# Kernel optimization log

Measured on AMD Instinct MI355X. Metric: run time of the kernel, lower is better.

Reference implementation:

```python
import jax, jax.numpy as jnp
import numpy as np
from jax import lax

B, S, K, H, NCLS = 64, 2048, 2, 256, 2
D = K * K  # input_dim = conv_kernel ** 2


def setup_inputs() -> dict:
    key = jax.random.key(0)
    ks = jax.random.split(key, 12)
    s = 0.1
    return {
        "x": jax.random.normal(ks[0], (B, S, D), dtype=jnp.float32),
        # elementwise quanvolution-style conv filter (k x k)
        "conv_w": jax.random.normal(ks[1], (K, K), dtype=jnp.float32) * s,
        "conv_b": jax.random.normal(ks[2], (K, K), dtype=jnp.float32) * s,
        # LSTM params, torch gate order (i, f, g, o)
        "w_ih": jax.random.normal(ks[3], (4 * H, D), dtype=jnp.float32) * s,
        "w_hh": jax.random.normal(ks[4], (4 * H, H), dtype=jnp.float32) * s,
        "b_ih": jax.random.normal(ks[5], (4 * H,), dtype=jnp.float32) * s,
        "b_hh": jax.random.normal(ks[6], (4 * H,), dtype=jnp.float32) * s,
        # classifier: depth=2 ReLU layers + final Linear(H, NCLS)
        "w1": jax.random.normal(ks[7], (H, H), dtype=jnp.float32) * s,
        "b1": jnp.zeros((H,), dtype=jnp.float32),
        "w2": jax.random.normal(ks[8], (H, H), dtype=jnp.float32) * s,
        "b2": jnp.zeros((H,), dtype=jnp.float32),
        "w3": jax.random.normal(ks[9], (NCLS, H), dtype=jnp.float32) * s,
        "b3": jnp.zeros((NCLS,), dtype=jnp.float32),
    }


def _lstm(feat, w_ih, w_hh, b_ih, b_hh):
    # feat: [B, S, D] -> hidden states [B, S, H]
    b, _, _ = feat.shape
    h_dim = w_hh.shape[1]
    bias = b_ih + b_hh
    # precompute input projections for all timesteps (batched GEMM)
    gates_x = jnp.einsum('bsd,gd->bsg', feat, w_ih) + bias  # [B, S, 4H]

    def step(carry, gx):
        h, c = carry
        gates = gx + h @ w_hh.T  # [B, 4H]
        i, f, g, o = jnp.split(gates, 4, axis=-1)
        i, f, o = jax.nn.sigmoid(i), jax.nn.sigmoid(f), jax.nn.sigmoid(o)
        g = jnp.tanh(g)
        c = f * c + i * g
        h = o * jnp.tanh(c)
        return (h, c), h

    init = (jnp.zeros((b, h_dim), feat.dtype), jnp.zeros((b, h_dim), feat.dtype))
    _, hs = lax.scan(step, init, gates_x.transpose(1, 0, 2))  # hs: [S, B, H]
    return hs.transpose(1, 0, 2)


def reference(x, conv_w, conv_b, w_ih, w_hh, b_ih, b_hh, w1, b1, w2, b2, w3, b3):
    b, s, _ = x.shape
    # batched replacement of the per-patch CPU conv loop
    patches = x.reshape(b, s, K, K)
    feat = jax.nn.sigmoid(patches * conv_w + conv_b).reshape(b, s, K * K)
    lstm_out = _lstm(feat, w_ih, w_hh, b_ih, b_hh)  # [B, S, H]
    h1 = jax.nn.relu(lstm_out @ w1.T + b1)
    h2 = jax.nn.relu(h1 @ w2.T + b2)
    logits = h2 @ w3.T + b3  # [B, S, NCLS]
    return logits
```

## Files before the change

kernel.cpp:

```cpp
#include <hip/hip_runtime.h>


#define BB 64
#define SS 2048
#define HH 256

typedef _Float16 f16;
typedef _Float16 h2 __attribute__((ext_vector_type(2)));
typedef _Float16 v8h __attribute__((ext_vector_type(8)));

union V8H { v8h v; h2 p[4]; };

__device__ __forceinline__ float fdot2f(h2 a, h2 b, float c){
#if __has_builtin(__builtin_amdgcn_fdot2)
  return __builtin_amdgcn_fdot2(a, b, c, false);
#else
  return c + (float)a.x*(float)b.x + (float)a.y*(float)b.y;
#endif
}

__device__ __forceinline__ float qsum4(float x){
#if __has_builtin(__builtin_amdgcn_mov_dpp)
  x += __int_as_float(__builtin_amdgcn_mov_dpp(__float_as_int(x), 0xB1, 0xf, 0xf, true));
  x += __int_as_float(__builtin_amdgcn_mov_dpp(__float_as_int(x), 0x4E, 0xf, 0xf, true));
#else
  x += __shfl_xor(x, 1, 64);
  x += __shfl_xor(x, 2, 64);
#endif
  return x;
}

__device__ __forceinline__ float rcpf_(float x){
#if __has_builtin(__builtin_amdgcn_rcpf)
  return __builtin_amdgcn_rcpf(x);
#else
  return 1.f/x;
#endif
}
__device__ __forceinline__ float sigmf_(float x){ return rcpf_(1.f + __expf(-x)); }
__device__ __forceinline__ float tanhf_(float x){
  x = fminf(fmaxf(x, -15.f), 15.f);
  float e = __expf(2.f*x);
  return (e - 1.f)*rcpf_(e + 1.f);
}
__device__ __forceinline__ h2 mkh2(float a, float b){ h2 r; r.x=(f16)a; r.y=(f16)b; return r; }

__device__ __forceinline__ void lds_barrier(){
  asm volatile("s_waitcnt lgkmcnt(0)\n\ts_barrier" ::: "memory");
}

__global__ void prep_kernel(
    const float* __restrict__ x, const float* __restrict__ conv_w, const float* __restrict__ conv_b,
    const float* __restrict__ w_ih, const float* __restrict__ w_hh,
    const float* __restrict__ b_ih, const float* __restrict__ b_hh,
    const float* __restrict__ w1, const float* __restrict__ w2, const float* __restrict__ w3,
    f16* __restrict__ feat2, f16* __restrict__ wstream, f16* __restrict__ wihp,
    float* __restrict__ biasp, f16* __restrict__ w1t, f16* __restrict__ w2t, f16* __restrict__ w3p)
{
  int id = blockIdx.x*256 + threadIdx.x;
  if (id < BB*SS){
    float4 xv = *(const float4*)(x + (size_t)id*4);
    float f0 = sigmf_(xv.x*conv_w[0] + conv_b[0]);
    float f1 = sigmf_(xv.y*conv_w[1] + conv_b[1]);
    float f2 = sigmf_(xv.z*conv_w[2] + conv_b[2]);
    float f3 = sigmf_(xv.w*conv_w[3] + conv_b[3]);
    h2* o = (h2*)feat2 + (size_t)id*2;
    o[0] = mkh2(f0,f1); o[1] = mkh2(f2,f3);
    return;
  }
  id -= BB*SS;
  if (id < 8192){
    int c = id >> 10, t = id & 1023;
    int u = t >> 2, kq = t & 3;
    int row = 768 + u;
    int j0 = kq*64 + c*8;
    const float* src = w_hh + (size_t)row*256 + j0;
    v8h o;
    #pragma unroll
    for (int j=0;j<8;j++) o[j] = (f16)src[j];
    *((v8h*)wstream + (size_t)c*1024 + t) = o;
    return;
  }
  id -= 8192;
  if (id < 1024){
    int u = id >> 2;
    f16* o = wihp + (size_t)id*16;
    float bb[4];
    #pragma unroll
    for (int i=0;i<4;i++){
      int row = u + 256*i;
      o[i*4+0] = (f16)w_ih[row*4+0];
      o[i*4+1] = (f16)w_ih[row*4+1];
      o[i*4+2] = (f16)w_ih[row*4+2];
      o[i*4+3] = (f16)w_ih[row*4+3];
      bb[i] = b_ih[row] + b_hh[row];
    }
    *(float4*)(biasp + (size_t)id*4) = make_float4(bb[0],bb[1],bb[2],bb[3]);
    return;
  }
  id -= 1024;
  if (id < 32768){
    int kp = id >> 8, n = id & 255;
    w1t[(size_t)id*2+0] = (f16)w1[(size_t)n*256 + 2*kp];
    w1t[(size_t)id*2+1] = (f16)w1[(size_t)n*256 + 2*kp+1];
    return;
  }
  id -= 32768;
  if (id < 32768){
    int kp = id >> 8, n = id & 255;
    w2t[(size_t)id*2+0] = (f16)w2[(size_t)n*256 + 2*kp];
    w2t[(size_t)id*2+1] = (f16)w2[(size_t)n*256 + 2*kp+1];
    return;
  }
  id -= 32768;
  if (id < 256){
    int kp = id >> 1, cls = id & 1;
    w3p[(size_t)id*2+0] = (f16)w3[(size_t)cls*256 + 2*kp];
    w3p[(size_t)id*2+1] = (f16)w3[(size_t)cls*256 + 2*kp+1];
  }
}

#define GSEG 9

__global__ __launch_bounds__(1024, 4) void lstm_kernel(
    const float* __restrict__ w_hh, const f16* __restrict__ feat2,
    const f16* __restrict__ wstream, const f16* __restrict__ wihp,
    const float* __restrict__ biasp, f16* __restrict__ hbuf)
{
  extern __shared__ __align__(16) f16 glds[];
  const int b = blockIdx.x, t = threadIdx.x;
  const int u = t >> 2, kq = t & 3;
  __shared__ __align__(16) f16 hsh[2][4][72];

  h2 wr0[32], wr1[32];
  {
    const float* s0 = w_hh + (size_t)u*256 + kq*64;
    const float* s1 = w_hh + (size_t)(u+256)*256 + kq*64;
    #pragma unroll
    for (int c=0;c<8;c++){
      float4 a = *(const float4*)(s0 + c*8);
      float4 q = *(const float4*)(s0 + c*8 + 4);
      wr0[c*4+0] = mkh2(a.x,a.y); wr0[c*4+1] = mkh2(a.z,a.w);
      wr0[c*4+2] = mkh2(q.x,q.y); wr0[c*4+3] = mkh2(q.z,q.w);
      a = *(const float4*)(s1 + c*8);
      q = *(const float4*)(s1 + c*8 + 4);
      wr1[c*4+0] = mkh2(a.x,a.y); wr1[c*4+1] = mkh2(a.z,a.w);
      wr1[c*4+2] = mkh2(q.x,q.y); wr1[c*4+3] = mkh2(q.z,q.w);
    }
  }
  {
    const float* gsrc = w_hh + (size_t)(512+u)*256 + kq*64;
    v8h* gdst = (v8h*)glds + (size_t)t*GSEG;
    #pragma unroll
    for (int c=0;c<8;c++){
      float4 a = *(const float4*)(gsrc + c*8);
      float4 q = *(const float4*)(gsrc + c*8 + 4);
      v8h o;
      o[0]=(f16)a.x; o[1]=(f16)a.y; o[2]=(f16)a.z; o[3]=(f16)a.w;
      o[4]=(f16)q.x; o[5]=(f16)q.y; o[6]=(f16)q.z; o[7]=(f16)q.w;
      gdst[c] = o;
    }
  }
  h2 wx[8];
  {
    const h2* p = (const h2*)(wihp + (size_t)t*16);
    #pragma unroll
    for (int j=0;j<8;j++) wx[j] = p[j];
  }
  const float4 bsv = *(const float4*)(biasp + (size_t)t*4);

  if (t < 256) hsh[0][t>>6][t&63] = (f16)0.f;
  __syncthreads();

  const v8h* wsp = (const v8h*)wstream + t;
  const v8h* gp  = (const v8h*)glds + (size_t)t*GSEG;
  const h2* fp = (const h2*)feat2 + (size_t)b*SS*2;
  f16* hrow = hbuf + (size_t)b*SS*HH;
  float cst = 0.f;
  int buf = 0;

  for (int s=0; s<SS; ++s){
    h2 f0 = fp[0], f1 = fp[1]; fp += 2;
    const v8h* hq = (const v8h*)(&hsh[buf][kq][0]);
    float a0=0.f, a1=0.f, a2=0.f, a3=0.f;
    #pragma unroll
    for (int c=0;c<8;c++){
      V8H wo; wo.v = wsp[(size_t)c*1024];
      V8H hv; hv.v = hq[c];
      V8H gv; gv.v = gp[c];
      h2 p0 = hv.p[0], p1 = hv.p[1], p2 = hv.p[2], p3 = hv.p[3];
      a0 = fdot2f(wr0[c*4+0], p0, a0); a0 = fdot2f(wr0[c*4+1], p1, a0);
      a0 = fdot2f(wr0[c*4+2], p2, a0); a0 = fdot2f(wr0[c*4+3], p3, a0);
      a1 = fdot2f(wr1[c*4+0], p0, a1); a1 = fdot2f(wr1[c*4+1], p1, a1);
      a1 = fdot2f(wr1[c*4+2], p2, a1); a1 = fdot2f(wr1[c*4+3], p3, a1);
      a2 = fdot2f(gv.p[0], p0, a2); a2 = fdot2f(gv.p[1], p1, a2);
      a2 = fdot2f(gv.p[2], p2, a2); a2 = fdot2f(gv.p[3], p3, a2);
      a3 = fdot2f(wo.p[0], p0, a3); a3 = fdot2f(wo.p[1], p1, a3);
      a3 = fdot2f(wo.p[2], p2, a3); a3 = fdot2f(wo.p[3], p3, a3);
    }
    a0 = qsum4(a0); a1 = qsum4(a1); a2 = qsum4(a2); a3 = qsum4(a3);
    float gi = fdot2f(wx[1], f1, fdot2f(wx[0], f0, a0 + bsv.x));
    float gf = fdot2f(wx[3], f1, fdot2f(wx[2], f0, a1 + bsv.y));
    float gg = fdot2f(wx[5], f1, fdot2f(wx[4], f0, a2 + bsv.z));
    float go = fdot2f(wx[7], f1, fdot2f(wx[6], f0, a3 + bsv.w));
    float iv = sigmf_(gi), fv = sigmf_(gf), gv2 = tanhf_(gg), ov = sigmf_(go);
    cst = fv*cst + iv*gv2;
    float hn = ov * tanhf_(cst);
    if (kq == 0){
      f16 hf = (f16)hn;
      hsh[buf^1][u>>6][u&63] = hf;
      hrow[u] = hf;
    }
    hrow += HH;
    lds_barrier();
    buf ^= 1;
  }
}

__device__ __forceinline__ void fc_layer(const h2 (*src)[16], h2 (*dst)[16],
                                         const f16* __restrict__ wt,
                                         const float* __restrict__ bias, int t)
{
  const int rg = t >> 6;
  const int c0 = (t & 63) * 4;
  float acc[4][4];
  #pragma unroll
  for (int r=0;r<4;r++){ acc[r][0]=0.f; acc[r][1]=0.f; acc[r][2]=0.f; acc[r][3]=0.f; }
  #pragma unroll 4
  for (int kp=0; kp<128; kp++){
    V8H wv; wv.v = *(const v8h*)(wt + ((size_t)kp*256 + c0)*2);
    V8H rv; rv.v = *(const v8h*)(&src[kp][rg*4]);
    #pragma unroll
    for (int r=0;r<4;r++)
      #pragma unroll
      for (int c=0;c<4;c++)
        acc[r][c] = fdot2f(rv.p[r], wv.p[c], acc[r][c]);
  }
  const float4 bv = *(const float4*)(bias + c0);
  #pragma unroll
  for (int r=0;r<4;r++){
    float o0 = fmaxf(acc[r][0]+bv.x, 0.f);
    float o1 = fmaxf(acc[r][1]+bv.y, 0.f);
    float o2 = fmaxf(acc[r][2]+bv.z, 0.f);
    float o3 = fmaxf(acc[r][3]+bv.w, 0.f);
    dst[(c0>>1)  ][rg*4+r] = mkh2(o0,o1);
    dst[(c0>>1)+1][rg*4+r] = mkh2(o2,o3);
  }
}

__global__ __launch_bounds__(256) void cls_kernel(
    const f16* __restrict__ hbuf, const f16* __restrict__ w1t, const f16* __restrict__ w2t,
    const f16* __restrict__ w3p, const float* __restrict__ b1, const float* __restrict__ b2,
    const float* __restrict__ b3, float* __restrict__ out)
{
  __shared__ __align__(16) h2 rlA[128][16];
  __shared__ __align__(16) h2 rlB[128][16];
  const int t = threadIdx.x;
  const size_t R = (size_t)blockIdx.x * 16;
  {
    int r = t >> 4, seg = t & 15;
    const v8h* src = (const v8h*)(hbuf + (R + r)*HH + seg*16);
    V8H aH; aH.v = src[0];
    V8H bH; bH.v = src[1];
    int kp0 = seg*8;
    #pragma unroll
    for (int j=0;j<4;j++) rlA[kp0+j  ][r] = aH.p[j];
    #pragma unroll
    for (int j=0;j<4;j++) rlA[kp0+4+j][r] = bH.p[j];
  }
  __syncthreads();
  fc_layer(rlA, rlB, w1t, b1, t);
  __syncthreads();
  fc_layer(rlB, rlA, w2t, b2, t);
  __syncthreads();
  if (t < 32){
    int r = t >> 1, cls = t & 1;
    float acc = b3[cls];
    const h2* w3h = (const h2*)w3p;
    #pragma unroll 8
    for (int kp=0; kp<128; kp++)
      acc = fdot2f(rlA[kp][r], w3h[kp*2 + cls], acc);
    out[(R + r)*2 + cls] = acc;
  }
}

extern "C" void kernel_launch(void* const* d_in, const int* in_sizes, int n_in,
                              void* d_out, int out_size, void* d_ws, size_t ws_size,
                              hipStream_t stream) {
  const float* x      = (const float*)d_in[0];
  const float* conv_w = (const float*)d_in[1];
  const float* conv_b = (const float*)d_in[2];
  const float* w_ih   = (const float*)d_in[3];
  const float* w_hh   = (const float*)d_in[4];
  const float* b_ih   = (const float*)d_in[5];
  const float* b_hh   = (const float*)d_in[6];
  const float* w1     = (const float*)d_in[7];
  const float* b1     = (const float*)d_in[8];
  const float* w2     = (const float*)d_in[9];
  const float* b2     = (const float*)d_in[10];
  const float* w3     = (const float*)d_in[11];
  const float* b3     = (const float*)d_in[12];

  char* ws = (char*)d_ws;
  f16*   feat2   = (f16*)  (ws + 0x000000);
  f16*   wstream = (f16*)  (ws + 0x100000);
  f16*   wihp    = (f16*)  (ws + 0x120000);
  float* biasp   = (float*)(ws + 0x128000);
  f16*   w1t     = (f16*)  (ws + 0x12C000);
  f16*   w2t     = (f16*)  (ws + 0x14C000);
  f16*   w3p     = (f16*)  (ws + 0x16C000);
  f16*   hbuf    = (f16*)  (ws + 0x170000);

  const int glds_bytes = 1024 * 72 * sizeof(f16);
  (void)hipFuncSetAttribute((const void*)lstm_kernel,
                            hipFuncAttributeMaxDynamicSharedMemorySize, glds_bytes);

  prep_kernel<<<805, 256, 0, stream>>>(x, conv_w, conv_b, w_ih, w_hh, b_ih, b_hh,
                                       w1, w2, w3,
                                       feat2, wstream, wihp, biasp, w1t, w2t, w3p);
  lstm_kernel<<<BB, 1024, glds_bytes, stream>>>(w_hh, feat2, wstream, wihp, biasp, hbuf);
  cls_kernel<<<(BB*SS)/16, 256, 0, stream>>>(hbuf, w1t, w2t, w3p, b1, b2, b3, (float*)d_out);
}
```

Before: 3.942 ms.

## Split LSTM recurrence over 512 threads with three gate weights in registers

The recurrent LSTM kernel now uses 512 threads per batch row, two threads per hidden unit, each covering half of the 256-wide K dimension. The i, f and o rows of w_hh are held in registers and the g rows in LDS, so the output-gate weights no longer have to be streamed from global memory every step. The cross-lane reduction drops from 4 lanes to 2. This cuts per-step global traffic and barrier width, but triples register weight storage per thread to roughly 192 VGPRs of weights, which risks spills and leaves fewer waves to hide latency.

```diff
diff --git a/kernel.cpp b/kernel.cpp
--- a/kernel.cpp
+++ b/kernel.cpp
@@ -19,13 +19,11 @@
 #endif
 }
 
-__device__ __forceinline__ float qsum4(float x){
+__device__ __forceinline__ float psum2(float x){
 #if __has_builtin(__builtin_amdgcn_mov_dpp)
   x += __int_as_float(__builtin_amdgcn_mov_dpp(__float_as_int(x), 0xB1, 0xf, 0xf, true));
-  x += __int_as_float(__builtin_amdgcn_mov_dpp(__float_as_int(x), 0x4E, 0xf, 0xf, true));
 #else
   x += __shfl_xor(x, 1, 64);
-  x += __shfl_xor(x, 2, 64);
 #endif
   return x;
 }
@@ -54,7 +52,7 @@
     const float* __restrict__ w_ih, const float* __restrict__ w_hh,
     const float* __restrict__ b_ih, const float* __restrict__ b_hh,
     const float* __restrict__ w1, const float* __restrict__ w2, const float* __restrict__ w3,
-    f16* __restrict__ feat2, f16* __restrict__ wstream, f16* __restrict__ wihp,
+    f16* __restrict__ feat2, f16* __restrict__ wihp,
     float* __restrict__ biasp, f16* __restrict__ w1t, f16* __restrict__ w2t, f16* __restrict__ w3p)
 {
   int id = blockIdx.x*256 + threadIdx.x;
@@ -69,19 +67,6 @@
     return;
   }
   id -= BB*SS;
-  if (id < 8192){
-    int c = id >> 10, t = id & 1023;
-    int u = t >> 2, kq = t & 3;
-    int row = 768 + u;
-    int j0 = kq*64 + c*8;
-    const float* src = w_hh + (size_t)row*256 + j0;
-    v8h o;
-    #pragma unroll
-    for (int j=0;j<8;j++) o[j] = (f16)src[j];
-    *((v8h*)wstream + (size_t)c*1024 + t) = o;
-    return;
-  }
-  id -= 8192;
   if (id < 1024){
     int u = id >> 2;
     f16* o = wihp + (size_t)id*16;
@@ -120,41 +105,46 @@
   }
 }
 
-#define GSEG 9
-
-__global__ __launch_bounds__(1024, 4) void lstm_kernel(
+#define GSEGV 17
+
+__global__ __launch_bounds__(512, 2) void lstm_kernel(
     const float* __restrict__ w_hh, const f16* __restrict__ feat2,
-    const f16* __restrict__ wstream, const f16* __restrict__ wihp,
-    const float* __restrict__ biasp, f16* __restrict__ hbuf)
+    const f16* __restrict__ wihp, const float* __restrict__ biasp,
+    f16* __restrict__ hbuf)
 {
   extern __shared__ __align__(16) f16 glds[];
   const int b = blockIdx.x, t = threadIdx.x;
-  const int u = t >> 2, kq = t & 3;
-  __shared__ __align__(16) f16 hsh[2][4][72];
-
-  h2 wr0[32], wr1[32];
+  const int u = t >> 1, hf = t & 1;
+  __shared__ __align__(16) f16 hsh[2][2][136];
+
+  h2 wi[64], wf[64], wo[64];
   {
-    const float* s0 = w_hh + (size_t)u*256 + kq*64;
-    const float* s1 = w_hh + (size_t)(u+256)*256 + kq*64;
-    #pragma unroll
-    for (int c=0;c<8;c++){
-      float4 a = *(const float4*)(s0 + c*8);
-      float4 q = *(const float4*)(s0 + c*8 + 4);
-      wr0[c*4+0] = mkh2(a.x,a.y); wr0[c*4+1] = mkh2(a.z,a.w);
-      wr0[c*4+2] = mkh2(q.x,q.y); wr0[c*4+3] = mkh2(q.z,q.w);
-      a = *(const float4*)(s1 + c*8);
-      q = *(const float4*)(s1 + c*8 + 4);
-      wr1[c*4+0] = mkh2(a.x,a.y); wr1[c*4+1] = mkh2(a.z,a.w);
-      wr1[c*4+2] = mkh2(q.x,q.y); wr1[c*4+3] = mkh2(q.z,q.w);
+    const float* si = w_hh + (size_t)u*256       + hf*128;
+    const float* sf = w_hh + (size_t)(u+256)*256 + hf*128;
+    const float* so = w_hh + (size_t)(u+768)*256 + hf*128;
+    #pragma unroll
+    for (int c=0;c<16;c++){
+      float4 a = *(const float4*)(si + c*8);
+      float4 q = *(const float4*)(si + c*8 + 4);
+      wi[c*4+0] = mkh2(a.x,a.y); wi[c*4+1] = mkh2(a.z,a.w);
+      wi[c*4+2] = mkh2(q.x,q.y); wi[c*4+3] = mkh2(q.z,q.w);
+      a = *(const float4*)(sf + c*8);
+      q = *(const float4*)(sf + c*8 + 4);
+      wf[c*4+0] = mkh2(a.x,a.y); wf[c*4+1] = mkh2(a.z,a.w);
+      wf[c*4+2] = mkh2(q.x,q.y); wf[c*4+3] = mkh2(q.z,q.w);
+      a = *(const float4*)(so + c*8);
+      q = *(const float4*)(so + c*8 + 4);
+      wo[c*4+0] = mkh2(a.x,a.y); wo[c*4+1] = mkh2(a.z,a.w);
+      wo[c*4+2] = mkh2(q.x,q.y); wo[c*4+3] = mkh2(q.z,q.w);
     }
   }
   {
-    const float* gsrc = w_hh + (size_t)(512+u)*256 + kq*64;
-    v8h* gdst = (v8h*)glds + (size_t)t*GSEG;
-    #pragma unroll
-    for (int c=0;c<8;c++){
-      float4 a = *(const float4*)(gsrc + c*8);
-      float4 q = *(const float4*)(gsrc + c*8 + 4);
+    const float* sg = w_hh + (size_t)(512+u)*256 + hf*128;
+    v8h* gdst = (v8h*)glds + (size_t)t*GSEGV;
+    #pragma unroll
+    for (int c=0;c<16;c++){
+      float4 a = *(const float4*)(sg + c*8);
+      float4 q = *(const float4*)(sg + c*8 + 4);
       v8h o;
       o[0]=(f16)a.x; o[1]=(f16)a.y; o[2]=(f16)a.z; o[3]=(f16)a.w;
       o[4]=(f16)q.x; o[5]=(f16)q.y; o[6]=(f16)q.z; o[7]=(f16)q.w;
@@ -163,17 +153,16 @@
   }
   h2 wx[8];
   {
-    const h2* p = (const h2*)(wihp + (size_t)t*16);
+    const h2* p = (const h2*)(wihp + (size_t)(t*2)*16);
     #pragma unroll
     for (int j=0;j<8;j++) wx[j] = p[j];
   }
-  const float4 bsv = *(const float4*)(biasp + (size_t)t*4);
-
-  if (t < 256) hsh[0][t>>6][t&63] = (f16)0.f;
+  const float4 bsv = *(const float4*)(biasp + (size_t)(t*2)*4);
+
+  if (t < 256) hsh[0][t>>7][t&127] = (f16)0.f;
   __syncthreads();
 
-  const v8h* wsp = (const v8h*)wstream + t;
-  const v8h* gp  = (const v8h*)glds + (size_t)t*GSEG;
+  const v8h* gp = (const v8h*)glds + (size_t)t*GSEGV;
   const h2* fp = (const h2*)feat2 + (size_t)b*SS*2;
   f16* hrow = hbuf + (size_t)b*SS*HH;
   float cst = 0.f;
@@ -181,24 +170,23 @@
 
   for (int s=0; s<SS; ++s){
     h2 f0 = fp[0], f1 = fp[1]; fp += 2;
-    const v8h* hq = (const v8h*)(&hsh[buf][kq][0]);
+    const v8h* hq = (const v8h*)(&hsh[buf][hf][0]);
     float a0=0.f, a1=0.f, a2=0.f, a3=0.f;
     #pragma unroll
-    for (int c=0;c<8;c++){
-      V8H wo; wo.v = wsp[(size_t)c*1024];
+    for (int c=0;c<16;c++){
       V8H hv; hv.v = hq[c];
       V8H gv; gv.v = gp[c];
       h2 p0 = hv.p[0], p1 = hv.p[1], p2 = hv.p[2], p3 = hv.p[3];
-      a0 = fdot2f(wr0[c*4+0], p0, a0); a0 = fdot2f(wr0[c*4+1], p1, a0);
-      a0 = fdot2f(wr0[c*4+2], p2, a0); a0 = fdot2f(wr0[c*4+3], p3, a0);
-      a1 = fdot2f(wr1[c*4+0], p0, a1); a1 = fdot2f(wr1[c*4+1], p1, a1);
-      a1 = fdot2f(wr1[c*4+2], p2, a1); a1 = fdot2f(wr1[c*4+3], p3, a1);
+      a0 = fdot2f(wi[c*4+0], p0, a0); a0 = fdot2f(wi[c*4+1], p1, a0);
+      a0 = fdot2f(wi[c*4+2], p2, a0); a0 = fdot2f(wi[c*4+3], p3, a0);
+      a1 = fdot2f(wf[c*4+0], p0, a1); a1 = fdot2f(wf[c*4+1], p1, a1);
+      a1 = fdot2f(wf[c*4+2], p2, a1); a1 = fdot2f(wf[c*4+3], p3, a1);
       a2 = fdot2f(gv.p[0], p0, a2); a2 = fdot2f(gv.p[1], p1, a2);
       a2 = fdot2f(gv.p[2], p2, a2); a2 = fdot2f(gv.p[3], p3, a2);
-      a3 = fdot2f(wo.p[0], p0, a3); a3 = fdot2f(wo.p[1], p1, a3);
-      a3 = fdot2f(wo.p[2], p2, a3); a3 = fdot2f(wo.p[3], p3, a3);
-    }
-    a0 = qsum4(a0); a1 = qsum4(a1); a2 = qsum4(a2); a3 = qsum4(a3);
+      a3 = fdot2f(wo[c*4+0], p0, a3); a3 = fdot2f(wo[c*4+1], p1, a3);
+      a3 = fdot2f(wo[c*4+2], p2, a3); a3 = fdot2f(wo[c*4+3], p3, a3);
+    }
+    a0 = psum2(a0); a1 = psum2(a1); a2 = psum2(a2); a3 = psum2(a3);
     float gi = fdot2f(wx[1], f1, fdot2f(wx[0], f0, a0 + bsv.x));
     float gf = fdot2f(wx[3], f1, fdot2f(wx[2], f0, a1 + bsv.y));
     float gg = fdot2f(wx[5], f1, fdot2f(wx[4], f0, a2 + bsv.z));
@@ -206,10 +194,10 @@
     float iv = sigmf_(gi), fv = sigmf_(gf), gv2 = tanhf_(gg), ov = sigmf_(go);
     cst = fv*cst + iv*gv2;
     float hn = ov * tanhf_(cst);
-    if (kq == 0){
-      f16 hf = (f16)hn;
-      hsh[buf^1][u>>6][u&63] = hf;
-      hrow[u] = hf;
+    if (hf == 0){
+      f16 hh = (f16)hn;
+      hsh[buf^1][u>>7][u&127] = hh;
+      hrow[u] = hh;
     }
     hrow += HH;
     lds_barrier();
@@ -303,21 +291,20 @@
 
   char* ws = (char*)d_ws;
   f16*   feat2   = (f16*)  (ws + 0x000000);
-  f16*   wstream = (f16*)  (ws + 0x100000);
-  f16*   wihp    = (f16*)  (ws + 0x120000);
-  float* biasp   = (float*)(ws + 0x128000);
-  f16*   w1t     = (f16*)  (ws + 0x12C000);
-  f16*   w2t     = (f16*)  (ws + 0x14C000);
-  f16*   w3p     = (f16*)  (ws + 0x16C000);
-  f16*   hbuf    = (f16*)  (ws + 0x170000);
-
-  const int glds_bytes = 1024 * 72 * sizeof(f16);
+  f16*   wihp    = (f16*)  (ws + 0x100000);
+  float* biasp   = (float*)(ws + 0x108000);
+  f16*   w1t     = (f16*)  (ws + 0x10C000);
+  f16*   w2t     = (f16*)  (ws + 0x12C000);
+  f16*   w3p     = (f16*)  (ws + 0x14C000);
+  f16*   hbuf    = (f16*)  (ws + 0x150000);
+
+  const int glds_bytes = 512 * GSEGV * 16;
   (void)hipFuncSetAttribute((const void*)lstm_kernel,
                             hipFuncAttributeMaxDynamicSharedMemorySize, glds_bytes);
 
-  prep_kernel<<<805, 256, 0, stream>>>(x, conv_w, conv_b, w_ih, w_hh, b_ih, b_hh,
+  prep_kernel<<<773, 256, 0, stream>>>(x, conv_w, conv_b, w_ih, w_hh, b_ih, b_hh,
                                        w1, w2, w3,
-                                       feat2, wstream, wihp, biasp, w1t, w2t, w3p);
-  lstm_kernel<<<BB, 1024, glds_bytes, stream>>>(w_hh, feat2, wstream, wihp, biasp, hbuf);
+                                       feat2, wihp, biasp, w1t, w2t, w3p);
+  lstm_kernel<<<BB, 512, glds_bytes, stream>>>(w_hh, feat2, wihp, biasp, hbuf);
   cls_kernel<<<(BB*SS)/16, 256, 0, stream>>>(hbuf, w1t, w2t, w3p, b1, b2, b3, (float*)d_out);
 }
```

Measured after the change: 3.367 ms. 1.17x faster.
